# Kernel optimization log

Measured on AMD Instinct MI355X. Metric: run time of the kernel, lower is better.

The kernel has to match this reference:

```python
import jax, jax.numpy as jnp
import numpy as np

B, M, T = 16, 256, 128
D, H, L, V = 512, 8, 4, 32000
BOS = 32000
HD = D // H
NEG = -1e9


def _ln(x, g, b, eps=1e-5):
    m = x.mean(-1, keepdims=True)
    v = ((x - m) ** 2).mean(-1, keepdims=True)
    return (x - m) / jnp.sqrt(v + eps) * g + b


def _split(t):  # [B,S,D] -> [B,H,S,HD]
    return t.reshape(t.shape[0], t.shape[1], H, HD).transpose(0, 2, 1, 3)


def _merge(t):  # [B,H,S,HD] -> [B,S,D]
    return t.transpose(0, 2, 1, 3).reshape(t.shape[0], t.shape[2], D)


def setup_inputs() -> dict:
    key = jax.random.key(0)
    ks = jax.random.split(key, 40)
    rn = lambda k, shape, s=0.02: jax.random.normal(k, shape, jnp.float32) * s
    inp = {
        'memory': jax.random.normal(ks[0], (B, M, D), jnp.float32),
        'targets': jax.random.randint(ks[1], (B, T), 0, V, jnp.int64),
        'tok_emb': rn(ks[2], (V + 1, D)),
        'pos_emb': rn(ks[3], (T + 1, D)),
        'sa_qkv_w': rn(ks[4], (L, D, 3 * D)), 'sa_qkv_b': jnp.zeros((L, 3 * D)),
        'sa_out_w': rn(ks[5], (L, D, D)), 'sa_out_b': jnp.zeros((L, D)),
        'ca_q_w': rn(ks[6], (L, D, D)), 'ca_q_b': jnp.zeros((L, D)),
        'ca_kv_w': rn(ks[7], (L, D, 2 * D)), 'ca_kv_b': jnp.zeros((L, 2 * D)),
        'ca_out_w': rn(ks[8], (L, D, D)), 'ca_out_b': jnp.zeros((L, D)),
        'ffn1_w': rn(ks[9], (L, D, 4 * D)), 'ffn1_b': jnp.zeros((L, 4 * D)),
        'ffn2_w': rn(ks[10], (L, 4 * D, D)), 'ffn2_b': jnp.zeros((L, D)),
        'ln1_g': jnp.ones((L, D)), 'ln1_b': jnp.zeros((L, D)),
        'ln2_g': jnp.ones((L, D)), 'ln2_b': jnp.zeros((L, D)),
        'ln3_g': jnp.ones((L, D)), 'ln3_b': jnp.zeros((L, D)),
        'normf_g': jnp.ones((D,)), 'normf_b': jnp.zeros((D,)),
        'out_w': rn(ks[11], (D, V)), 'out_b': jnp.zeros((V,)),
    }
    return inp


def reference(memory, targets, tok_emb, pos_emb, sa_qkv_w, sa_qkv_b, sa_out_w,
              sa_out_b, ca_q_w, ca_q_b, ca_kv_w, ca_kv_b, ca_out_w, ca_out_b,
              ffn1_w, ffn1_b, ffn2_w, ffn2_b, ln1_g, ln1_b, ln2_g, ln2_b,
              ln3_g, ln3_b, normf_g, normf_b, out_w, out_b):
    # teacher forcing: prepend BOS, drop last target token
    bos = jnp.full((memory.shape[0], 1), BOS, dtype=targets.dtype)
    inp = jnp.concatenate([bos, targets[:, :-1]], axis=1)  # [B,T]
    S = inp.shape[1]
    x = tok_emb[inp] + pos_emb[jnp.arange(S)][None]  # [B,T,D]
    causal = jnp.tril(jnp.ones((S, S), bool))
    scale = 1.0 / np.sqrt(HD)
    for l in range(L):
        # self-attention (pre-norm)
        h = _ln(x, ln1_g[l], ln1_b[l])
        q, k, v = jnp.split(h @ sa_qkv_w[l] + sa_qkv_b[l], 3, axis=-1)
        q, k, v = _split(q), _split(k), _split(v)
        s = jnp.einsum('bhqd,bhkd->bhqk', q, k) * scale
        a = jax.nn.softmax(jnp.where(causal, s, NEG), axis=-1)
        x = x + _merge(jnp.einsum('bhqk,bhkd->bhqd', a, v)) @ sa_out_w[l] + sa_out_b[l]
        # cross-attention to memory
        h = _ln(x, ln2_g[l], ln2_b[l])
        q = _split(h @ ca_q_w[l] + ca_q_b[l])
        k, v = jnp.split(memory @ ca_kv_w[l] + ca_kv_b[l], 2, axis=-1)
        k, v = _split(k), _split(v)
        s = jnp.einsum('bhqd,bhkd->bhqk', q, k) * scale
        a = jax.nn.softmax(s, axis=-1)
        x = x + _merge(jnp.einsum('bhqk,bhkd->bhqd', a, v)) @ ca_out_w[l] + ca_out_b[l]
        # FFN (gelu, exact erf form as torch 'gelu')
        h = _ln(x, ln3_g[l], ln3_b[l])
        x = x + jax.nn.gelu(h @ ffn1_w[l] + ffn1_b[l], approximate=False) @ ffn2_w[l] + ffn2_b[l]
    x = _ln(x, normf_g, normf_b)
    return x @ out_w + out_b  # [B,T,V]
```

## Files before the change

kernel.cpp:

```cpp
#include <hip/hip_runtime.h>
#include <hip/hip_bf16.h>
#include <math.h>

#define BB 16
#define TT 128
#define MM 256
#define DD 512
#define HH 8
#define LL 4
#define VV 32000
#define BOS_TOK 32000

typedef __attribute__((ext_vector_type(8))) short s8v;
typedef __attribute__((ext_vector_type(4))) float f4v;

__device__ __forceinline__ float bs2f(short u) {
    union { unsigned int i; float f; } c;
    c.i = ((unsigned int)(unsigned short)u) << 16;
    return c.f;
}
__device__ __forceinline__ short f2bs(float f) {
    union { float f; unsigned int u; } c;
    c.f = f;
    unsigned int r = (c.u + 0x7FFFu + ((c.u >> 16) & 1u)) >> 16;
    return (short)r;
}

__global__ __launch_bounds__(256) void cvt_k(const float* __restrict__ src,
                                             short* __restrict__ dst, int n4) {
    int i = (blockIdx.x * 256 + threadIdx.x);
    if (i < n4) {
        f4v v = *(const f4v*)&src[i * 4];
#pragma unroll
        for (int j = 0; j < 4; j++) dst[i * 4 + j] = f2bs(v[j]);
    }
}

__global__ __launch_bounds__(256) void wt_k(const float* __restrict__ src,
                                            short* __restrict__ dst, int K, int N) {
    __shared__ short t[64][65];
    int k0 = blockIdx.x * 64, n0 = blockIdx.y * 64;
    size_t zo = (size_t)blockIdx.z * K * N;
    int tid = threadIdx.x;
    int kr = tid >> 2;
    int nc = (tid & 3) * 16;
    const float* sp = src + zo + (size_t)(k0 + kr) * N + n0 + nc;
#pragma unroll
    for (int c = 0; c < 4; c++) {
        f4v v = *(const f4v*)(sp + c * 4);
#pragma unroll
        for (int j = 0; j < 4; j++) t[kr][nc + c * 4 + j] = f2bs(v[j]);
    }
    __syncthreads();
    int nr = tid >> 2;
    int kc = (tid & 3) * 16;
    short* dp = dst + zo + (size_t)(n0 + nr) * K + k0 + kc;
#pragma unroll
    for (int c = 0; c < 2; c++) {
        s8v v;
#pragma unroll
        for (int j = 0; j < 8; j++) v[j] = t[kc + c * 8 + j][nr];
        *(s8v*)(dp + c * 8) = v;
    }
}

__global__ __launch_bounds__(256) void embed_k(const int* __restrict__ tgt,
                                               const float* __restrict__ tok,
                                               const float* __restrict__ pos,
                                               float* __restrict__ X) {
    int row = blockIdx.x;
    int t = row & (TT - 1);
    int b = row >> 7;
    int idx = (t == 0) ? BOS_TOK : tgt[b * TT + t - 1];
    const float* te = tok + (size_t)idx * DD;
    const float* pe = pos + (size_t)t * DD;
    float* xr = X + (size_t)row * DD;
    for (int d = threadIdx.x; d < DD; d += 256)
        xr[d] = te[d] + pe[d];
}

__global__ __launch_bounds__(256) void ln_k(const float* __restrict__ X,
                                            const float* __restrict__ g,
                                            const float* __restrict__ bta,
                                            short* __restrict__ H) {
    int row = blockIdx.x;
    int tid = threadIdx.x;
    const float* xr = X + (size_t)row * DD;
    float v0 = xr[tid], v1 = xr[tid + 256];
    float s = v0 + v1, ss = v0 * v0 + v1 * v1;
    for (int o = 32; o; o >>= 1) {
        s += __shfl_xor(s, o, 64);
        ss += __shfl_xor(ss, o, 64);
    }
    __shared__ float r0[4], r1[4];
    int wave = tid >> 6, lane = tid & 63;
    if (lane == 0) { r0[wave] = s; r1[wave] = ss; }
    __syncthreads();
    s = r0[0] + r0[1] + r0[2] + r0[3];
    ss = r1[0] + r1[1] + r1[2] + r1[3];
    float mean = s * (1.0f / DD);
    float var = ss * (1.0f / DD) - mean * mean;
    float rstd = rsqrtf(var + 1e-5f);
    short* hr = H + (size_t)row * DD;
    hr[tid] = f2bs((v0 - mean) * rstd * g[tid] + bta[tid]);
    hr[tid + 256] = f2bs((v1 - mean) * rstd * g[tid + 256] + bta[tid + 256]);
}

template <int EPI, int BM, int BN>
__global__ __launch_bounds__(256) void gemm_k(const short* __restrict__ A,
                                              const short* __restrict__ Bt,
                                              const float* __restrict__ bias,
                                              short* __restrict__ C,
                                              float* __restrict__ X, int M, int N, int K) {
    constexpr int MI = BM / 32;
    constexpr int NJ = BN / 32;
    __shared__ short Al[BM * 34];
    __shared__ short Bl[BN * 34];
    int tid = threadIdx.x, lane = tid & 63, wave = tid >> 6;
    int wm = wave >> 1, wn = wave & 1;
    int quad = lane >> 4, l16 = lane & 15;

    int nwg = gridDim.x * gridDim.y;
    int orig = blockIdx.y * gridDim.x + blockIdx.x;
    int q = nwg >> 3, r = nwg & 7;
    int xcd = orig & 7, pos = orig >> 3;
    int wg = (xcd < r ? xcd * (q + 1) : r * (q + 1) + (xcd - r) * q) + pos;
    int mt = wg % gridDim.x, nt = wg / gridDim.x;
    int m0 = mt * BM, n0 = nt * BN;

    f4v acc[MI][NJ];
#pragma unroll
    for (int i = 0; i < MI; i++)
#pragma unroll
        for (int j = 0; j < NJ; j++) acc[i][j] = (f4v){0.f, 0.f, 0.f, 0.f};

    constexpr int TPRA = 256 / BM;
    constexpr int CA = 32 / TPRA;
    int arow = tid / TPRA, acol = (tid % TPRA) * CA;
    constexpr int TPRB = 256 / BN;
    constexpr int CB = 32 / TPRB;
    int brow = tid / TPRB, bcol = (tid % TPRB) * CB;

    for (int k0 = 0; k0 < K; k0 += 32) {
#pragma unroll
        for (int c = 0; c < CA / 8; c++)
            *(s8v*)&Al[arow * 34 + acol + c * 8] =
                *(const s8v*)&A[(size_t)(m0 + arow) * K + k0 + acol + c * 8];
#pragma unroll
        for (int c = 0; c < CB / 8; c++)
            *(s8v*)&Bl[brow * 34 + bcol + c * 8] =
                *(const s8v*)&Bt[(size_t)(n0 + brow) * K + k0 + bcol + c * 8];
        __syncthreads();
        s8v af[MI], bf[NJ];
#pragma unroll
        for (int i = 0; i < MI; i++)
            af[i] = *(const s8v*)&Al[(wm * (BM / 2) + 16 * i + l16) * 34 + quad * 8];
#pragma unroll
        for (int j = 0; j < NJ; j++)
            bf[j] = *(const s8v*)&Bl[(wn * (BN / 2) + 16 * j + l16) * 34 + quad * 8];
#pragma unroll
        for (int i = 0; i < MI; i++)
#pragma unroll
            for (int j = 0; j < NJ; j++)
                acc[i][j] = __builtin_amdgcn_mfma_f32_16x16x32_bf16(af[i], bf[j], acc[i][j], 0, 0, 0);
        __syncthreads();
    }
#pragma unroll
    for (int i = 0; i < MI; i++) {
#pragma unroll
        for (int j = 0; j < NJ; j++) {
            int gc = n0 + wn * (BN / 2) + 16 * j + l16;
            float bz = bias[gc];
#pragma unroll
            for (int r2 = 0; r2 < 4; r2++) {
                int gr = m0 + wm * (BM / 2) + 16 * i + quad * 4 + r2;
                float v = acc[i][j][r2] + bz;
                if (EPI == 1) v = 0.5f * v * (1.0f + erff(v * 0.70710678118f));
                if (EPI == 2) {
                    size_t o = (size_t)gr * N + gc;
                    X[o] = X[o] + v;
                } else if (EPI == 3) {
                    X[(size_t)gr * N + gc] = v;
                } else {
                    C[(size_t)gr * N + gc] = f2bs(v);
                }
            }
        }
    }
}

template <int EPI>
__global__ __launch_bounds__(256) void gemm_w32_k(const short* __restrict__ A,
                                                  const float* __restrict__ W,
                                                  const float* __restrict__ bias,
                                                  short* __restrict__ C,
                                                  float* __restrict__ X, int M, int N, int K) {
    __shared__ short Al[64 * 32];
    __shared__ short Bl[32 * 66];
    int tid = threadIdx.x, lane = tid & 63, wave = tid >> 6;
    int wm = wave >> 1, wn = wave & 1;
    int quad = lane >> 4, l16 = lane & 15;
    int m0 = blockIdx.y * 64, n0 = blockIdx.x * 64;
    f4v acc[2][2];
#pragma unroll
    for (int i = 0; i < 2; i++)
#pragma unroll
        for (int j = 0; j < 2; j++) acc[i][j] = (f4v){0.f, 0.f, 0.f, 0.f};
    int arow = tid >> 2, acol = (tid & 3) * 8;
    int brow = tid >> 3, bcol = (tid & 7) * 8;
    for (int k0 = 0; k0 < K; k0 += 32) {
        *(s8v*)&Al[arow * 32 + acol] = *(const s8v*)&A[(size_t)(m0 + arow) * K + k0 + acol];
        const float* wp = &W[(size_t)(k0 + brow) * N + n0 + bcol];
        f4v wa = *(const f4v*)wp;
        f4v wb = *(const f4v*)(wp + 4);
#pragma unroll
        for (int j = 0; j < 4; j++) {
            Bl[brow * 66 + bcol + j] = f2bs(wa[j]);
            Bl[brow * 66 + bcol + 4 + j] = f2bs(wb[j]);
        }
        __syncthreads();
        s8v af[2], bf[2];
#pragma unroll
        for (int i = 0; i < 2; i++)
            af[i] = *(const s8v*)&Al[(32 * wm + 16 * i + l16) * 32 + quad * 8];
#pragma unroll
        for (int j = 0; j < 2; j++) {
            s8v t;
#pragma unroll
            for (int u = 0; u < 8; u++)
                t[u] = Bl[(quad * 8 + u) * 66 + 32 * wn + 16 * j + l16];
            bf[j] = t;
        }
#pragma unroll
        for (int i = 0; i < 2; i++)
#pragma unroll
            for (int j = 0; j < 2; j++)
                acc[i][j] = __builtin_amdgcn_mfma_f32_16x16x32_bf16(af[i], bf[j], acc[i][j], 0, 0, 0);
        __syncthreads();
    }
#pragma unroll
    for (int i = 0; i < 2; i++) {
#pragma unroll
        for (int j = 0; j < 2; j++) {
            int gc = n0 + 32 * wn + 16 * j + l16;
            float bz = bias[gc];
#pragma unroll
            for (int r = 0; r < 4; r++) {
                int gr = m0 + 32 * wm + 16 * i + quad * 4 + r;
                float v = acc[i][j][r] + bz;
                if (EPI == 1) v = 0.5f * v * (1.0f + erff(v * 0.70710678118f));
                if (EPI == 2) {
                    size_t o = (size_t)gr * N + gc;
                    X[o] = X[o] + v;
                } else if (EPI == 3) {
                    X[(size_t)gr * N + gc] = v;
                } else {
                    C[(size_t)gr * N + gc] = f2bs(v);
                }
            }
        }
    }
}

template <int NK>
__device__ __forceinline__ void sattn_body(const short* __restrict__ qkv,
                                           short* __restrict__ attn,
                                           short* Ql, short* Kl, short* Vt, short* Pl,
                                           int b, int h) {
    constexpr int QBASE = NK - 64;
    constexpr int NJ = NK / 16;
    constexpr int QS = 72, KS = 72, VS = NK + 8, PS = NK + 8;
    int tid = threadIdx.x, lane = tid & 63, wave = tid >> 6;
    int quad = lane >> 4, l16 = lane & 15;
    size_t baseq = ((size_t)b * TT + QBASE) * 1536 + h * 64;
    size_t basek = ((size_t)b * TT) * 1536 + 512 + h * 64;
    size_t basev = basek + 512;
    {
        int row = tid >> 2, c = (tid & 3) * 16;
        *(s8v*)&Ql[row * QS + c] = *(const s8v*)&qkv[baseq + (size_t)row * 1536 + c];
        *(s8v*)&Ql[row * QS + c + 8] = *(const s8v*)&qkv[baseq + (size_t)row * 1536 + c + 8];
    }
    for (int idx = tid; idx < NK * 4; idx += 256) {
        int row = idx >> 2, c = (idx & 3) * 16;
        *(s8v*)&Kl[row * KS + c] = *(const s8v*)&qkv[basek + (size_t)row * 1536 + c];
        *(s8v*)&Kl[row * KS + c + 8] = *(const s8v*)&qkv[basek + (size_t)row * 1536 + c + 8];
    }
    for (int idx = tid; idx < NK * 4; idx += 256) {
        int key = idx >> 2, c = (idx & 3) * 16;
        s8v v0 = *(const s8v*)&qkv[basev + (size_t)key * 1536 + c];
        s8v v1 = *(const s8v*)&qkv[basev + (size_t)key * 1536 + c + 8];
#pragma unroll
        for (int u = 0; u < 8; u++) {
            Vt[(c + u) * VS + key] = v0[u];
            Vt[(c + 8 + u) * VS + key] = v1[u];
        }
    }
    __syncthreads();
    s8v af[2];
#pragma unroll
    for (int kc = 0; kc < 2; kc++)
        af[kc] = *(const s8v*)&Ql[(wave * 16 + l16) * QS + kc * 32 + quad * 8];
    f4v s[NJ];
#pragma unroll
    for (int j = 0; j < NJ; j++) s[j] = (f4v){0.f, 0.f, 0.f, 0.f};
#pragma unroll
    for (int j = 0; j < NJ; j++) {
#pragma unroll
        for (int kc = 0; kc < 2; kc++) {
            s8v bf = *(const s8v*)&Kl[(j * 16 + l16) * KS + kc * 32 + quad * 8];
            s[j] = __builtin_amdgcn_mfma_f32_16x16x32_bf16(af[kc], bf, s[j], 0, 0, 0);
        }
    }
    float sum[4];
#pragma unroll
    for (int r = 0; r < 4; r++) {
        int grow = QBASE + wave * 16 + quad * 4 + r;
        float m = -1e30f;
#pragma unroll
        for (int j = 0; j < NJ; j++) {
            int col = j * 16 + l16;
            float v = (col <= grow) ? s[j][r] * 0.125f : -1e30f;
            s[j][r] = v;
            m = fmaxf(m, v);
        }
        for (int o = 8; o; o >>= 1) m = fmaxf(m, __shfl_xor(m, o, 64));
        float sm = 0.f;
#pragma unroll
        for (int j = 0; j < NJ; j++) {
            float e = expf(s[j][r] - m);
            s[j][r] = e;
            sm += e;
        }
        for (int o = 8; o; o >>= 1) sm += __shfl_xor(sm, o, 64);
        sum[r] = sm;
    }
#pragma unroll
    for (int j = 0; j < NJ; j++)
#pragma unroll
        for (int r = 0; r < 4; r++)
            Pl[(wave * 16 + quad * 4 + r) * PS + j * 16 + l16] = f2bs(s[j][r]);
    __syncthreads();
    f4v o[4];
#pragma unroll
    for (int j2 = 0; j2 < 4; j2++) o[j2] = (f4v){0.f, 0.f, 0.f, 0.f};
#pragma unroll
    for (int kc = 0; kc < NK / 32; kc++) {
        s8v pa = *(const s8v*)&Pl[(wave * 16 + l16) * PS + kc * 32 + quad * 8];
#pragma unroll
        for (int j2 = 0; j2 < 4; j2++) {
            s8v bv = *(const s8v*)&Vt[(j2 * 16 + l16) * VS + kc * 32 + quad * 8];
            o[j2] = __builtin_amdgcn_mfma_f32_16x16x32_bf16(pa, bv, o[j2], 0, 0, 0);
        }
    }
    float inv[4];
#pragma unroll
    for (int r = 0; r < 4; r++) inv[r] = 1.0f / sum[r];
#pragma unroll
    for (int j2 = 0; j2 < 4; j2++)
#pragma unroll
        for (int r = 0; r < 4; r++) {
            int grow = QBASE + wave * 16 + quad * 4 + r;
            attn[((size_t)b * TT + grow) * DD + h * 64 + j2 * 16 + l16] = f2bs(o[j2][r] * inv[r]);
        }
}

__global__ __launch_bounds__(256) void sattn_m(const short* __restrict__ qkv,
                                               short* __restrict__ attn) {
    __shared__ short Ql[64 * 72];
    __shared__ short Kl[128 * 72];
    __shared__ short Vt[64 * 136];
    __shared__ short Pl[64 * 136];
    int bh = blockIdx.x;
    int b = bh >> 3, h = bh & 7;
    if (blockIdx.y == 0)
        sattn_body<64>(qkv, attn, Ql, Kl, Vt, Pl, b, h);
    else
        sattn_body<128>(qkv, attn, Ql, Kl, Vt, Pl, b, h);
}

__global__ __launch_bounds__(256) void cattn_m(const short* __restrict__ qb,
                                               const short* __restrict__ kvb,
                                               short* __restrict__ attn) {
    constexpr int NJ = 16;
    constexpr int QS = 72, KS = 72, VS = 264, PS = 264;
    __shared__ short Ql[64 * QS];
    __shared__ short Kl[256 * KS];
    __shared__ short Vt[64 * VS];
    __shared__ short Pl[64 * PS];
    int bh = blockIdx.x, grp = blockIdx.y;
    int b = bh >> 3, h = bh & 7;
    int tid = threadIdx.x, lane = tid & 63, wave = tid >> 6;
    int quad = lane >> 4, l16 = lane & 15;
    size_t baseq = ((size_t)b * TT + grp * 64) * DD + h * 64;
    size_t basek = ((size_t)b * MM) * 1024 + h * 64;
    size_t basev = basek + 512;
    {
        int row = tid >> 2, c = (tid & 3) * 16;
        *(s8v*)&Ql[row * QS + c] = *(const s8v*)&qb[baseq + (size_t)row * DD + c];
        *(s8v*)&Ql[row * QS + c + 8] = *(const s8v*)&qb[baseq + (size_t)row * DD + c + 8];
    }
    for (int idx = tid; idx < 256 * 4; idx += 256) {
        int row = idx >> 2, c = (idx & 3) * 16;
        *(s8v*)&Kl[row * KS + c] = *(const s8v*)&kvb[basek + (size_t)row * 1024 + c];
        *(s8v*)&Kl[row * KS + c + 8] = *(const s8v*)&kvb[basek + (size_t)row * 1024 + c + 8];
    }
    for (int idx = tid; idx < 256 * 4; idx += 256) {
        int key = idx >> 2, c = (idx & 3) * 16;
        s8v v0 = *(const s8v*)&kvb[basev + (size_t)key * 1024 + c];
        s8v v1 = *(const s8v*)&kvb[basev + (size_t)key * 1024 + c + 8];
#pragma unroll
        for (int u = 0; u < 8; u++) {
            Vt[(c + u) * VS + key] = v0[u];
            Vt[(c + 8 + u) * VS + key] = v1[u];
        }
    }
    __syncthreads();
    s8v af[2];
#pragma unroll
    for (int kc = 0; kc < 2; kc++)
        af[kc] = *(const s8v*)&Ql[(wave * 16 + l16) * QS + kc * 32 + quad * 8];
    f4v s[NJ];
#pragma unroll
    for (int j = 0; j < NJ; j++) s[j] = (f4v){0.f, 0.f, 0.f, 0.f};
#pragma unroll
    for (int j = 0; j < NJ; j++) {
#pragma unroll
        for (int kc = 0; kc < 2; kc++) {
            s8v bf = *(const s8v*)&Kl[(j * 16 + l16) * KS + kc * 32 + quad * 8];
            s[j] = __builtin_amdgcn_mfma_f32_16x16x32_bf16(af[kc], bf, s[j], 0, 0, 0);
        }
    }
    float sum[4];
#pragma unroll
    for (int r = 0; r < 4; r++) {
        float m = -1e30f;
#pragma unroll
        for (int j = 0; j < NJ; j++) {
            float v = s[j][r] * 0.125f;
            s[j][r] = v;
            m = fmaxf(m, v);
        }
        for (int o = 8; o; o >>= 1) m = fmaxf(m, __shfl_xor(m, o, 64));
        float sm = 0.f;
#pragma unroll
        for (int j = 0; j < NJ; j++) {
            float e = expf(s[j][r] - m);
            s[j][r] = e;
            sm += e;
        }
        for (int o = 8; o; o >>= 1) sm += __shfl_xor(sm, o, 64);
        sum[r] = sm;
    }
#pragma unroll
    for (int j = 0; j < NJ; j++)
#pragma unroll
        for (int r = 0; r < 4; r++)
            Pl[(wave * 16 + quad * 4 + r) * PS + j * 16 + l16] = f2bs(s[j][r]);
    __syncthreads();
    f4v o[4];
#pragma unroll
    for (int j2 = 0; j2 < 4; j2++) o[j2] = (f4v){0.f, 0.f, 0.f, 0.f};
#pragma unroll
    for (int kc = 0; kc < 8; kc++) {
        s8v pa = *(const s8v*)&Pl[(wave * 16 + l16) * PS + kc * 32 + quad * 8];
#pragma unroll
        for (int j2 = 0; j2 < 4; j2++) {
            s8v bv = *(const s8v*)&Vt[(j2 * 16 + l16) * VS + kc * 32 + quad * 8];
            o[j2] = __builtin_amdgcn_mfma_f32_16x16x32_bf16(pa, bv, o[j2], 0, 0, 0);
        }
    }
    float inv[4];
#pragma unroll
    for (int r = 0; r < 4; r++) inv[r] = 1.0f / sum[r];
#pragma unroll
    for (int j2 = 0; j2 < 4; j2++)
#pragma unroll
        for (int r = 0; r < 4; r++) {
            int grow = grp * 64 + wave * 16 + quad * 4 + r;
            attn[((size_t)b * TT + grow) * DD + h * 64 + j2 * 16 + l16] = f2bs(o[j2][r] * inv[r]);
        }
}

extern "C" void kernel_launch(void* const* d_in, const int* in_sizes, int n_in, void* d_out,
                              int out_size, void* d_ws, size_t ws_size, hipStream_t stream) {
    (void)in_sizes; (void)n_in; (void)out_size;
    typedef const float* fp;
    fp memory = (fp)d_in[0];
    const int* targets = (const int*)d_in[1];
    fp tok = (fp)d_in[2];
    fp pos = (fp)d_in[3];
    fp saqkv_w = (fp)d_in[4], saqkv_b = (fp)d_in[5];
    fp saout_w = (fp)d_in[6], saout_b = (fp)d_in[7];
    fp caq_w = (fp)d_in[8], caq_b = (fp)d_in[9];
    fp cakv_w = (fp)d_in[10], cakv_b = (fp)d_in[11];
    fp caout_w = (fp)d_in[12], caout_b = (fp)d_in[13];
    fp f1w = (fp)d_in[14], f1b = (fp)d_in[15];
    fp f2w = (fp)d_in[16], f2bb = (fp)d_in[17];
    fp ln1g = (fp)d_in[18], ln1b = (fp)d_in[19];
    fp ln2g = (fp)d_in[20], ln2b = (fp)d_in[21];
    fp ln3g = (fp)d_in[22], ln3b = (fp)d_in[23];
    fp lnfg = (fp)d_in[24], lnfb = (fp)d_in[25];
    fp outw = (fp)d_in[26], outb = (fp)d_in[27];
    float* out = (float*)d_out;

    char* ws = (char*)d_ws;
    float* X = (float*)ws;
    short* Hb = (short*)(ws + (4u << 20));
    short* ATT = (short*)(ws + (6u << 20));
    short* MEMB = (short*)(ws + (8u << 20));
    short* QKV = (short*)(ws + (12u << 20));
    short* Qb = (short*)(ws + (12u << 20));
    short* KVb = (short*)(ws + (14u << 20));
    short* F1 = (short*)(ws + (12u << 20));

    size_t wo = (size_t)22u << 20;
    short* WTqkv = (short*)(ws + wo);
    short* WTso  = (short*)(ws + wo + 6291456u);
    short* WTcq  = (short*)(ws + wo + 8388608u);
    short* WTckv = (short*)(ws + wo + 10485760u);
    short* WTco  = (short*)(ws + wo + 14680064u);
    short* WTf1  = (short*)(ws + wo + 16777216u);
    short* WTf2  = (short*)(ws + wo + 25165824u);
    short* WTout = (short*)(ws + wo + 33554432u);
    const size_t WS_NEED = wo + 33554432u + 32768000u;

    const int R = BB * TT;
    cvt_k<<<(BB * MM * DD / 4 + 255) / 256, 256, 0, stream>>>(memory, MEMB, BB * MM * DD / 4);
    embed_k<<<R, 256, 0, stream>>>(targets, tok, pos, X);

    if (ws_size >= WS_NEED) {
        wt_k<<<dim3(8, 24, LL), 256, 0, stream>>>(saqkv_w, WTqkv, DD, 1536);
        wt_k<<<dim3(8, 8, LL), 256, 0, stream>>>(saout_w, WTso, DD, DD);
        wt_k<<<dim3(8, 8, LL), 256, 0, stream>>>(caq_w, WTcq, DD, DD);
        wt_k<<<dim3(8, 16, LL), 256, 0, stream>>>(cakv_w, WTckv, DD, 1024);
        wt_k<<<dim3(8, 8, LL), 256, 0, stream>>>(caout_w, WTco, DD, DD);
        wt_k<<<dim3(8, 32, LL), 256, 0, stream>>>(f1w, WTf1, DD, 2048);
        wt_k<<<dim3(32, 8, LL), 256, 0, stream>>>(f2w, WTf2, 2048, DD);
        wt_k<<<dim3(8, 500, 1), 256, 0, stream>>>(outw, WTout, DD, VV);

        for (int l = 0; l < LL; l++) {
            ln_k<<<R, 256, 0, stream>>>(X, ln1g + l * DD, ln1b + l * DD, Hb);
            gemm_k<0, 128, 64><<<dim3(R / 128, 1536 / 64), 256, 0, stream>>>(
                Hb, WTqkv + (size_t)l * 1536 * DD, saqkv_b + l * 1536, QKV, nullptr, R, 1536, DD);
            sattn_m<<<dim3(BB * HH, 2), 256, 0, stream>>>(QKV, ATT);
            gemm_k<2, 64, 64><<<dim3(R / 64, DD / 64), 256, 0, stream>>>(
                ATT, WTso + (size_t)l * DD * DD, saout_b + l * DD, nullptr, X, R, DD, DD);
            ln_k<<<R, 256, 0, stream>>>(X, ln2g + l * DD, ln2b + l * DD, Hb);
            gemm_k<0, 64, 64><<<dim3(R / 64, DD / 64), 256, 0, stream>>>(
                Hb, WTcq + (size_t)l * DD * DD, caq_b + l * DD, Qb, nullptr, R, DD, DD);
            gemm_k<0, 128, 128><<<dim3((BB * MM) / 128, 1024 / 128), 256, 0, stream>>>(
                MEMB, WTckv + (size_t)l * 1024 * DD, cakv_b + l * 1024, KVb, nullptr, BB * MM, 1024, DD);
            cattn_m<<<dim3(BB * HH, 2), 256, 0, stream>>>(Qb, KVb, ATT);
            gemm_k<2, 64, 64><<<dim3(R / 64, DD / 64), 256, 0, stream>>>(
                ATT, WTco + (size_t)l * DD * DD, caout_b + l * DD, nullptr, X, R, DD, DD);
            ln_k<<<R, 256, 0, stream>>>(X, ln3g + l * DD, ln3b + l * DD, Hb);
            gemm_k<1, 128, 128><<<dim3(R / 128, 2048 / 128), 256, 0, stream>>>(
                Hb, WTf1 + (size_t)l * 2048 * DD, f1b + l * 2048, F1, nullptr, R, 2048, DD);
            gemm_k<2, 64, 64><<<dim3(R / 64, DD / 64), 256, 0, stream>>>(
                F1, WTf2 + (size_t)l * DD * 2048, f2bb + l * DD, nullptr, X, R, DD, 2048);
        }
        ln_k<<<R, 256, 0, stream>>>(X, lnfg, lnfb, Hb);
        gemm_k<3, 128, 128><<<dim3(R / 128, VV / 128), 256, 0, stream>>>(
            Hb, WTout, outb, nullptr, out, R, VV, DD);
    } else {
        for (int l = 0; l < LL; l++) {
            ln_k<<<R, 256, 0, stream>>>(X, ln1g + l * DD, ln1b + l * DD, Hb);
            gemm_w32_k<0><<<dim3(1536 / 64, R / 64), 256, 0, stream>>>(
                Hb, saqkv_w + (size_t)l * DD * 1536, saqkv_b + l * 1536, QKV, nullptr, R, 1536, DD);
            sattn_m<<<dim3(BB * HH, 2), 256, 0, stream>>>(QKV, ATT);
            gemm_w32_k<2><<<dim3(DD / 64, R / 64), 256, 0, stream>>>(
                ATT, saout_w + (size_t)l * DD * DD, saout_b + l * DD, nullptr, X, R, DD, DD);
            ln_k<<<R, 256, 0, stream>>>(X, ln2g + l * DD, ln2b + l * DD, Hb);
            gemm_w32_k<0><<<dim3(DD / 64, R / 64), 256, 0, stream>>>(
                Hb, caq_w + (size_t)l * DD * DD, caq_b + l * DD, Qb, nullptr, R, DD, DD);
            gemm_w32_k<0><<<dim3(1024 / 64, (BB * MM) / 64), 256, 0, stream>>>(
                MEMB, cakv_w + (size_t)l * DD * 1024, cakv_b + l * 1024, KVb, nullptr, BB * MM, 1024, DD);
            cattn_m<<<dim3(BB * HH, 2), 256, 0, stream>>>(Qb, KVb, ATT);
            gemm_w32_k<2><<<dim3(DD / 64, R / 64), 256, 0, stream>>>(
                ATT, caout_w + (size_t)l * DD * DD, caout_b + l * DD, nullptr, X, R, DD, DD);
            ln_k<<<R, 256, 0, stream>>>(X, ln3g + l * DD, ln3b + l * DD, Hb);
            gemm_w32_k<1><<<dim3(2048 / 64, R / 64), 256, 0, stream>>>(
                Hb, f1w + (size_t)l * DD * 2048, f1b + l * 2048, F1, nullptr, R, 2048, DD);
            gemm_w32_k<2><<<dim3(DD / 64, R / 64), 256, 0, stream>>>(
                F1, f2w + (size_t)l * 2048 * DD, f2bb + l * DD, nullptr, X, R, DD, 2048);
        }
        ln_k<<<R, 256, 0, stream>>>(X, lnfg, lnfb, Hb);
        gemm_w32_k<3><<<dim3(VV / 64, R / 64), 256, 0, stream>>>(Hb, outw, outb, nullptr, out, R, VV, DD);
    }
}
```

Baseline: 1.176 ms.

## Fuse layernorm into GEMM A-loads, double-buffer LDS, batch weight transposes

Removes the separate layernorm kernels. Each consuming GEMM now either computes per-row mean and rstd itself from the fp32 residual, or reads them from a small stats kernel for the vocab projection, and normalizes while staging A into LDS. The GEMM main loop becomes register-prefetched and double-buffered in LDS, which removes one barrier per k-step. The eight weight-transpose launches are merged into a single launch driven by a descriptor table. The trade-off is that A is now read in fp32 and g/bta are fetched per element, and each column tile recomputes the row stats.

```diff
diff --git a/kernel.cpp b/kernel.cpp
--- a/kernel.cpp
+++ b/kernel.cpp
@@ -36,11 +36,22 @@
     }
 }
 
-__global__ __launch_bounds__(256) void wt_k(const float* __restrict__ src,
-                                            short* __restrict__ dst, int K, int N) {
+struct WtDesc { const float* src; short* dst; int K, N, tpz, base, end, pad; };
+struct WtAll { WtDesc d[8]; };
+
+__global__ __launch_bounds__(256) void wt_all_k(WtAll wa) {
     __shared__ short t[64][65];
-    int k0 = blockIdx.x * 64, n0 = blockIdx.y * 64;
-    size_t zo = (size_t)blockIdx.z * K * N;
+    int linear = blockIdx.x;
+    int i = 0;
+    while (i < 7 && linear >= wa.d[i].end) i++;
+    const float* src = wa.d[i].src;
+    short* dst = wa.d[i].dst;
+    int K = wa.d[i].K, N = wa.d[i].N;
+    int rem = linear - wa.d[i].base;
+    int z = rem / wa.d[i].tpz, tl = rem % wa.d[i].tpz;
+    int nkt = K >> 6;
+    int k0 = (tl % nkt) * 64, n0 = (tl / nkt) * 64;
+    size_t zo = (size_t)z * K * N;
     int tid = threadIdx.x;
     int kr = tid >> 2;
     int nc = (tid & 3) * 16;
@@ -106,16 +117,41 @@
     hr[tid + 256] = f2bs((v1 - mean) * rstd * g[tid + 256] + bta[tid + 256]);
 }
 
-template <int EPI, int BM, int BN>
-__global__ __launch_bounds__(256) void gemm_k(const short* __restrict__ A,
+__global__ __launch_bounds__(256) void lnstat_k(const float* __restrict__ X,
+                                                float* __restrict__ st) {
+    int row = blockIdx.x * 4 + (threadIdx.x >> 6);
+    int lane = threadIdx.x & 63;
+    const float* xr = X + (size_t)row * DD + lane * 8;
+    f4v a = *(const f4v*)xr, b = *(const f4v*)(xr + 4);
+    float s = 0.f, ss = 0.f;
+#pragma unroll
+    for (int j = 0; j < 4; j++) { s += a[j] + b[j]; ss += a[j] * a[j] + b[j] * b[j]; }
+    for (int o = 32; o; o >>= 1) {
+        s += __shfl_xor(s, o, 64);
+        ss += __shfl_xor(ss, o, 64);
+    }
+    if (lane == 0) {
+        float mean = s * (1.0f / DD);
+        float var = ss * (1.0f / DD) - mean * mean;
+        st[row * 2] = mean;
+        st[row * 2 + 1] = rsqrtf(var + 1e-5f);
+    }
+}
+
+template <int EPI, int BM, int BN, int LNA>
+__global__ __launch_bounds__(256) void gemm_k(const void* __restrict__ Ain,
                                               const short* __restrict__ Bt,
                                               const float* __restrict__ bias,
                                               short* __restrict__ C,
-                                              float* __restrict__ X, int M, int N, int K) {
+                                              float* __restrict__ X, int M, int N, int K,
+                                              const float* __restrict__ g,
+                                              const float* __restrict__ bta,
+                                              const float* __restrict__ stats) {
     constexpr int MI = BM / 32;
     constexpr int NJ = BN / 32;
-    __shared__ short Al[BM * 34];
-    __shared__ short Bl[BN * 34];
+    __shared__ short Al[2][BM * 34];
+    __shared__ short Bl[2][BN * 34];
+    __shared__ float mu[BM], rs[BM];
     int tid = threadIdx.x, lane = tid & 63, wave = tid >> 6;
     int wm = wave >> 1, wn = wave & 1;
     int quad = lane >> 4, l16 = lane & 15;
@@ -128,12 +164,6 @@
     int mt = wg % gridDim.x, nt = wg / gridDim.x;
     int m0 = mt * BM, n0 = nt * BN;
 
-    f4v acc[MI][NJ];
-#pragma unroll
-    for (int i = 0; i < MI; i++)
-#pragma unroll
-        for (int j = 0; j < NJ; j++) acc[i][j] = (f4v){0.f, 0.f, 0.f, 0.f};
-
     constexpr int TPRA = 256 / BM;
     constexpr int CA = 32 / TPRA;
     int arow = tid / TPRA, acol = (tid % TPRA) * CA;
@@ -141,29 +171,112 @@
     constexpr int CB = 32 / TPRB;
     int brow = tid / TPRB, bcol = (tid % TPRB) * CB;
 
-    for (int k0 = 0; k0 < K; k0 += 32) {
-#pragma unroll
-        for (int c = 0; c < CA / 8; c++)
-            *(s8v*)&Al[arow * 34 + acol + c * 8] =
-                *(const s8v*)&A[(size_t)(m0 + arow) * K + k0 + acol + c * 8];
+    float mean_r = 0.f, rstd_r = 0.f;
+    if constexpr (LNA == 1) {
+        constexpr int TPR = 256 / BM;
+        int srow = tid / TPR, sseg = tid % TPR;
+        const float* xr = (const float*)Ain + (size_t)(m0 + srow) * DD + sseg * (DD / TPR);
+        float s = 0.f, ss = 0.f;
+#pragma unroll 8
+        for (int c = 0; c < DD / TPR / 4; c++) {
+            f4v v = *(const f4v*)(xr + c * 4);
+#pragma unroll
+            for (int j = 0; j < 4; j++) { s += v[j]; ss += v[j] * v[j]; }
+        }
+#pragma unroll
+        for (int o = TPR >> 1; o; o >>= 1) {
+            s += __shfl_xor(s, o, 64);
+            ss += __shfl_xor(ss, o, 64);
+        }
+        if (sseg == 0) {
+            float mean = s * (1.0f / DD);
+            float var = ss * (1.0f / DD) - mean * mean;
+            mu[srow] = mean;
+            rs[srow] = rsqrtf(var + 1e-5f);
+        }
+        __syncthreads();
+        mean_r = mu[arow];
+        rstd_r = rs[arow];
+    }
+    if constexpr (LNA == 2) {
+        mean_r = stats[(size_t)(m0 + arow) * 2];
+        rstd_r = stats[(size_t)(m0 + arow) * 2 + 1];
+    }
+
+    s8v ra16[CA / 8 > 0 ? CA / 8 : 1];
+    f4v raf[CA / 4];
+    s8v rb[CB / 8 > 0 ? CB / 8 : 1];
+
+    auto LOADA_ = [&](int k0) {
+        if constexpr (LNA == 0) {
+            const short* Ab = (const short*)Ain;
+#pragma unroll
+            for (int c = 0; c < CA / 8; c++)
+                ra16[c] = *(const s8v*)&Ab[(size_t)(m0 + arow) * K + k0 + acol + c * 8];
+        } else {
+            const float* Af = (const float*)Ain;
+#pragma unroll
+            for (int c = 0; c < CA / 4; c++)
+                raf[c] = *(const f4v*)&Af[(size_t)(m0 + arow) * DD + k0 + acol + c * 4];
+        }
+    };
+    auto STOREA_ = [&](int buf, int k0) {
+        if constexpr (LNA == 0) {
+#pragma unroll
+            for (int c = 0; c < CA / 8; c++)
+                *(s8v*)&Al[buf][arow * 34 + acol + c * 8] = ra16[c];
+        } else {
+#pragma unroll
+            for (int c = 0; c < CA / 4; c++)
+#pragma unroll
+                for (int j = 0; j < 4; j++) {
+                    int col = k0 + acol + c * 4 + j;
+                    Al[buf][arow * 34 + acol + c * 4 + j] =
+                        f2bs((raf[c][j] - mean_r) * rstd_r * g[col] + bta[col]);
+                }
+        }
+    };
+    auto LOADB_ = [&](int k0) {
 #pragma unroll
         for (int c = 0; c < CB / 8; c++)
-            *(s8v*)&Bl[brow * 34 + bcol + c * 8] =
-                *(const s8v*)&Bt[(size_t)(n0 + brow) * K + k0 + bcol + c * 8];
+            rb[c] = *(const s8v*)&Bt[(size_t)(n0 + brow) * K + k0 + bcol + c * 8];
+    };
+    auto STOREB_ = [&](int buf) {
+#pragma unroll
+        for (int c = 0; c < CB / 8; c++)
+            *(s8v*)&Bl[buf][brow * 34 + bcol + c * 8] = rb[c];
+    };
+
+    f4v acc[MI][NJ];
+#pragma unroll
+    for (int i = 0; i < MI; i++)
+#pragma unroll
+        for (int j = 0; j < NJ; j++) acc[i][j] = (f4v){0.f, 0.f, 0.f, 0.f};
+
+    LOADA_(0);
+    LOADB_(0);
+    STOREA_(0, 0);
+    STOREB_(0);
+    int nk = K / 32;
+    int cur = 0;
+    for (int t = 0; t < nk; t++) {
         __syncthreads();
+        int k0n = (t + 1) * 32;
+        bool pf = (t + 1 < nk);
+        if (pf) { LOADA_(k0n); LOADB_(k0n); }
         s8v af[MI], bf[NJ];
 #pragma unroll
         for (int i = 0; i < MI; i++)
-            af[i] = *(const s8v*)&Al[(wm * (BM / 2) + 16 * i + l16) * 34 + quad * 8];
+            af[i] = *(const s8v*)&Al[cur][(wm * (BM / 2) + 16 * i + l16) * 34 + quad * 8];
 #pragma unroll
         for (int j = 0; j < NJ; j++)
-            bf[j] = *(const s8v*)&Bl[(wn * (BN / 2) + 16 * j + l16) * 34 + quad * 8];
+            bf[j] = *(const s8v*)&Bl[cur][(wn * (BN / 2) + 16 * j + l16) * 34 + quad * 8];
 #pragma unroll
         for (int i = 0; i < MI; i++)
 #pragma unroll
             for (int j = 0; j < NJ; j++)
                 acc[i][j] = __builtin_amdgcn_mfma_f32_16x16x32_bf16(af[i], bf[j], acc[i][j], 0, 0, 0);
-        __syncthreads();
+        if (pf) { STOREA_(cur ^ 1, k0n); STOREB_(cur ^ 1); cur ^= 1; }
     }
 #pragma unroll
     for (int i = 0; i < MI; i++) {
@@ -506,6 +619,7 @@
     char* ws = (char*)d_ws;
     float* X = (float*)ws;
     short* Hb = (short*)(ws + (4u << 20));
+    float* ST = (float*)(ws + (4u << 20));
     short* ATT = (short*)(ws + (6u << 20));
     short* MEMB = (short*)(ws + (8u << 20));
     short* QKV = (short*)(ws + (12u << 20));
@@ -529,39 +643,53 @@
     embed_k<<<R, 256, 0, stream>>>(targets, tok, pos, X);
 
     if (ws_size >= WS_NEED) {
-        wt_k<<<dim3(8, 24, LL), 256, 0, stream>>>(saqkv_w, WTqkv, DD, 1536);
-        wt_k<<<dim3(8, 8, LL), 256, 0, stream>>>(saout_w, WTso, DD, DD);
-        wt_k<<<dim3(8, 8, LL), 256, 0, stream>>>(caq_w, WTcq, DD, DD);
-        wt_k<<<dim3(8, 16, LL), 256, 0, stream>>>(cakv_w, WTckv, DD, 1024);
-        wt_k<<<dim3(8, 8, LL), 256, 0, stream>>>(caout_w, WTco, DD, DD);
-        wt_k<<<dim3(8, 32, LL), 256, 0, stream>>>(f1w, WTf1, DD, 2048);
-        wt_k<<<dim3(32, 8, LL), 256, 0, stream>>>(f2w, WTf2, 2048, DD);
-        wt_k<<<dim3(8, 500, 1), 256, 0, stream>>>(outw, WTout, DD, VV);
+        WtAll wa;
+        int base = 0, idx = 0;
+        auto addw = [&](const float* s, short* d, int K, int N, int nz) {
+            int tpz = (K / 64) * (N / 64);
+            wa.d[idx].src = s; wa.d[idx].dst = d;
+            wa.d[idx].K = K; wa.d[idx].N = N; wa.d[idx].tpz = tpz;
+            wa.d[idx].base = base; base += tpz * nz; wa.d[idx].end = base;
+            wa.d[idx].pad = 0; idx++;
+        };
+        addw(saqkv_w, WTqkv, DD, 1536, LL);
+        addw(saout_w, WTso, DD, DD, LL);
+        addw(caq_w, WTcq, DD, DD, LL);
+        addw(cakv_w, WTckv, DD, 1024, LL);
+        addw(caout_w, WTco, DD, DD, LL);
+        addw(f1w, WTf1, DD, 2048, LL);
+        addw(f2w, WTf2, 2048, DD, LL);
+        addw(outw, WTout, DD, VV, 1);
+        wt_all_k<<<base, 256, 0, stream>>>(wa);
 
         for (int l = 0; l < LL; l++) {
-            ln_k<<<R, 256, 0, stream>>>(X, ln1g + l * DD, ln1b + l * DD, Hb);
-            gemm_k<0, 128, 64><<<dim3(R / 128, 1536 / 64), 256, 0, stream>>>(
-                Hb, WTqkv + (size_t)l * 1536 * DD, saqkv_b + l * 1536, QKV, nullptr, R, 1536, DD);
+            gemm_k<0, 128, 64, 1><<<dim3(R / 128, 1536 / 64), 256, 0, stream>>>(
+                X, WTqkv + (size_t)l * 1536 * DD, saqkv_b + l * 1536, QKV, nullptr, R, 1536, DD,
+                ln1g + l * DD, ln1b + l * DD, nullptr);
             sattn_m<<<dim3(BB * HH, 2), 256, 0, stream>>>(QKV, ATT);
-            gemm_k<2, 64, 64><<<dim3(R / 64, DD / 64), 256, 0, stream>>>(
-                ATT, WTso + (size_t)l * DD * DD, saout_b + l * DD, nullptr, X, R, DD, DD);
-            ln_k<<<R, 256, 0, stream>>>(X, ln2g + l * DD, ln2b + l * DD, Hb);
-            gemm_k<0, 64, 64><<<dim3(R / 64, DD / 64), 256, 0, stream>>>(
-                Hb, WTcq + (size_t)l * DD * DD, caq_b + l * DD, Qb, nullptr, R, DD, DD);
-            gemm_k<0, 128, 128><<<dim3((BB * MM) / 128, 1024 / 128), 256, 0, stream>>>(
-                MEMB, WTckv + (size_t)l * 1024 * DD, cakv_b + l * 1024, KVb, nullptr, BB * MM, 1024, DD);
+            gemm_k<2, 64, 64, 0><<<dim3(R / 64, DD / 64), 256, 0, stream>>>(
+                ATT, WTso + (size_t)l * DD * DD, saout_b + l * DD, nullptr, X, R, DD, DD,
+                nullptr, nullptr, nullptr);
+            gemm_k<0, 64, 64, 1><<<dim3(R / 64, DD / 64), 256, 0, stream>>>(
+                X, WTcq + (size_t)l * DD * DD, caq_b + l * DD, Qb, nullptr, R, DD, DD,
+                ln2g + l * DD, ln2b + l * DD, nullptr);
+            gemm_k<0, 128, 128, 0><<<dim3((BB * MM) / 128, 1024 / 128), 256, 0, stream>>>(
+                MEMB, WTckv + (size_t)l * 1024 * DD, cakv_b + l * 1024, KVb, nullptr, BB * MM, 1024, DD,
+                nullptr, nullptr, nullptr);
             cattn_m<<<dim3(BB * HH, 2), 256, 0, stream>>>(Qb, KVb, ATT);
-            gemm_k<2, 64, 64><<<dim3(R / 64, DD / 64), 256, 0, stream>>>(
-                ATT, WTco + (size_t)l * DD * DD, caout_b + l * DD, nullptr, X, R, DD, DD);
-            ln_k<<<R, 256, 0, stream>>>(X, ln3g + l * DD, ln3b + l * DD, Hb);
-            gemm_k<1, 128, 128><<<dim3(R / 128, 2048 / 128), 256, 0, stream>>>(
-                Hb, WTf1 + (size_t)l * 2048 * DD, f1b + l * 2048, F1, nullptr, R, 2048, DD);
-            gemm_k<2, 64, 64><<<dim3(R / 64, DD / 64), 256, 0, stream>>>(
-                F1, WTf2 + (size_t)l * DD * 2048, f2bb + l * DD, nullptr, X, R, DD, 2048);
-        }
-        ln_k<<<R, 256, 0, stream>>>(X, lnfg, lnfb, Hb);
-        gemm_k<3, 128, 128><<<dim3(R / 128, VV / 128), 256, 0, stream>>>(
-            Hb, WTout, outb, nullptr, out, R, VV, DD);
+            gemm_k<2, 64, 64, 0><<<dim3(R / 64, DD / 64), 256, 0, stream>>>(
+                ATT, WTco + (size_t)l * DD * DD, caout_b + l * DD, nullptr, X, R, DD, DD,
+                nullptr, nullptr, nullptr);
+            gemm_k<1, 128, 128, 1><<<dim3(R / 128, 2048 / 128), 256, 0, stream>>>(
+                X, WTf1 + (size_t)l * 2048 * DD, f1b + l * 2048, F1, nullptr, R, 2048, DD,
+                ln3g + l * DD, ln3b + l * DD, nullptr);
+            gemm_k<2, 64, 64, 0><<<dim3(R / 64, DD / 64), 256, 0, stream>>>(
+                F1, WTf2 + (size_t)l * DD * 2048, f2bb + l * DD, nullptr, X, R, DD, 2048,
+                nullptr, nullptr, nullptr);
+        }
+        lnstat_k<<<R / 4, 256, 0, stream>>>(X, ST);
+        gemm_k<3, 128, 128, 2><<<dim3(R / 128, VV / 128), 256, 0, stream>>>(
+            X, WTout, outb, nullptr, out, R, VV, DD, lnfg, lnfb, ST);
     } else {
         for (int l = 0; l < LL; l++) {
             ln_k<<<R, 256, 0, stream>>>(X, ln1g + l * DD, ln1b + l * DD, Hb);
```

Result: slower. 1.284 ms (+9.1%).
